# Optimization experiments

Measured on AMD Instinct MI355X. Metric: run time of the kernel, lower is better.

The kernel has to match this reference:

```python
import jax, jax.numpy as jnp
import numpy as np

DIM = 768
N_HEADS = 12
HEAD_DIM = DIM // N_HEADS
B, S = 2, 4096


def setup_inputs() -> dict:
    key = jax.random.key(0)
    k_x, k_wqkv, k_bqkv, k_wout, k_bout = jax.random.split(key, 5)
    scale_in = 1.0 / np.sqrt(DIM)
    return {
        "x": jax.random.normal(k_x, (B, S, DIM), dtype=jnp.float32),
        "Wqkv": jax.random.normal(k_wqkv, (DIM, 3 * DIM), dtype=jnp.float32) * scale_in,
        "bqkv": jax.random.normal(k_bqkv, (3 * DIM,), dtype=jnp.float32) * 0.02,
        "Wout": jax.random.normal(k_wout, (DIM, DIM), dtype=jnp.float32) * scale_in,
        "bout": jax.random.normal(k_bout, (DIM,), dtype=jnp.float32) * 0.02,
    }


def reference(x, Wqkv, bqkv, Wout, bout):
    b, s, d = x.shape
    qkv = (x @ Wqkv + bqkv).reshape(b, s, 3, N_HEADS, HEAD_DIM)
    qkv = jnp.transpose(qkv, (2, 0, 3, 1, 4))  # [3, B, H, S, hd]
    q, k, v = qkv[0], qkv[1], qkv[2]
    scale = HEAD_DIM ** -0.5
    attn = jnp.einsum('bhqd,bhkd->bhqk', q, k) * scale  # [B, H, S, S]
    causal_mask = jnp.triu(jnp.ones((s, s), dtype=bool), k=1)
    attn = jnp.where(causal_mask[None, None], -jnp.inf, attn)
    attn = jax.nn.softmax(attn, axis=-1)
    out = jnp.einsum('bhqk,bhkd->bhqd', attn, v)  # [B, H, S, hd]
    out = jnp.transpose(out, (0, 2, 1, 3)).reshape(b, s, d)
    return out @ Wout + bout
```

## Files before the change

kernel.cpp:

```cpp
#include <hip/hip_runtime.h>
#include <hip/hip_bf16.h>
#include <math.h>

#define DIM 768
#define NH 12
#define HD 64
#define BATCH 2
#define SEQ 4096
#define MTOT (BATCH * SEQ)

#define QSCALE 0.1803368801111244f

typedef unsigned short u16;
typedef __bf16 bf16x8 __attribute__((ext_vector_type(8)));
typedef float  f32x4  __attribute__((ext_vector_type(4)));
typedef unsigned short u16x4 __attribute__((ext_vector_type(4)));
typedef unsigned short u16x8 __attribute__((ext_vector_type(8)));

__device__ inline u16 f2bf(float f) {
    unsigned u = __builtin_bit_cast(unsigned, f);
    u += 0x7fffu + ((u >> 16) & 1u);
    return (u16)(u >> 16);
}

#if defined(__has_builtin) && __has_builtin(__builtin_amdgcn_cvt_pk_bf16_f32)
#define HAVE_PK_BF16 1
__device__ inline unsigned pk2bf(float a, float b) {
    auto v = __builtin_amdgcn_cvt_pk_bf16_f32(a, b);
    return __builtin_bit_cast(unsigned, v);
}
#else
#define HAVE_PK_BF16 0
__device__ inline unsigned pk2bf(float a, float b) {
    return (unsigned)f2bf(a) | ((unsigned)f2bf(b) << 16);
}
#endif

__device__ inline f32x4 mfma16(bf16x8 a, bf16x8 b, f32x4 c) {
    return __builtin_amdgcn_mfma_f32_16x16x32_bf16(a, b, c, 0, 0, 0);
}

__device__ inline void gl2lds16(const u16* g, u16* l) {
    __builtin_amdgcn_global_load_lds(
        (const __attribute__((address_space(1))) void*)g,
        (__attribute__((address_space(3))) void*)l,
        16, 0, 0);
}

__global__ __launch_bounds__(256)
void cvt_bf16(const float* __restrict__ src, u16* __restrict__ dst, int n8)
{
    int i = blockIdx.x * 256 + threadIdx.x;
    if (i >= n8) return;
    float4 a = ((const float4*)src)[i * 2];
    float4 b = ((const float4*)src)[i * 2 + 1];
    u16x8 o;
    o[0] = f2bf(a.x); o[1] = f2bf(a.y); o[2] = f2bf(a.z); o[3] = f2bf(a.w);
    o[4] = f2bf(b.x); o[5] = f2bf(b.y); o[6] = f2bf(b.z); o[7] = f2bf(b.w);
    ((u16x8*)dst)[i] = o;
}

__global__ __launch_bounds__(256)
void transpose_to_bf16(const float* __restrict__ src, u16* __restrict__ dst,
                       int R, int C)
{
    __shared__ float tile[32][33];
    const int c0 = blockIdx.x * 32, r0 = blockIdx.y * 32;
    const int tx = threadIdx.x & 31, ty = threadIdx.x >> 5;
#pragma unroll
    for (int i = 0; i < 4; ++i) {
        int row = ty * 4 + i;
        tile[row][tx] = src[(size_t)(r0 + row) * C + c0 + tx];
    }
    __syncthreads();
#pragma unroll
    for (int i = 0; i < 4; ++i) {
        int crow = ty * 4 + i;
        dst[(size_t)(c0 + crow) * R + r0 + tx] = f2bf(tile[tx][crow]);
    }
}

__device__ inline void gemm_lds_mainloop(const u16* __restrict__ Ag,
                                         const u16* __restrict__ Bg,
                                         int m0, int n0, int w, int lane,
                                         u16 (*As)[64 * 64], u16 (*Bs)[64 * 64],
                                         f32x4 acc[4][4])
{
    const int quad = lane >> 4, lc = lane & 15;
    const int wm = (w & 1) * 64, wn = (w >> 1) * 64;
    const int drow = lane >> 3;
    const int dp   = lane & 7;

#pragma unroll
    for (int mi = 0; mi < 4; ++mi)
#pragma unroll
        for (int nj = 0; nj < 4; ++nj)
            acc[mi][nj] = f32x4{0.f, 0.f, 0.f, 0.f};

#pragma unroll
    for (int i = 0; i < 2; ++i) {
        const int r  = w * 16 + i * 8 + drow;
        const int g  = dp ^ (r & 7);
        const int tr = 2 * r + (g >> 2);
        const int kc = g & 3;
        gl2lds16(Ag + (size_t)(m0 + tr) * 768 + kc * 8, &As[0][(w * 16 + i * 8) * 64]);
        gl2lds16(Bg + (size_t)(n0 + tr) * 768 + kc * 8, &Bs[0][(w * 16 + i * 8) * 64]);
    }
    __syncthreads();

    for (int ks = 0; ks < 24; ++ks) {
        const int cur = ks & 1;

        if (ks < 23) {
            const int k0n = (ks + 1) * 32;
#pragma unroll
            for (int i = 0; i < 2; ++i) {
                const int r  = w * 16 + i * 8 + drow;
                const int g  = dp ^ (r & 7);
                const int tr = 2 * r + (g >> 2);
                const int kc = g & 3;
                gl2lds16(Ag + (size_t)(m0 + tr) * 768 + k0n + kc * 8,
                         &As[1 - cur][(w * 16 + i * 8) * 64]);
                gl2lds16(Bg + (size_t)(n0 + tr) * 768 + k0n + kc * 8,
                         &Bs[1 - cur][(w * 16 + i * 8) * 64]);
            }
        }

        bf16x8 af[4], bfr[4];
#pragma unroll
        for (int mi = 0; mi < 4; ++mi) {
            const int m = wm + mi * 16 + lc;
            const int r = m >> 1;
            const int p = (((m & 1) * 4 + quad)) ^ (r & 7);
            af[mi] = *(const bf16x8*)&As[cur][r * 64 + p * 8];
        }
#pragma unroll
        for (int nj = 0; nj < 4; ++nj) {
            const int n = wn + nj * 16 + lc;
            const int r = n >> 1;
            const int p = (((n & 1) * 4 + quad)) ^ (r & 7);
            bfr[nj] = *(const bf16x8*)&Bs[cur][r * 64 + p * 8];
        }

#pragma unroll
        for (int mi = 0; mi < 4; ++mi)
#pragma unroll
            for (int nj = 0; nj < 4; ++nj)
                acc[mi][nj] = mfma16(af[mi], bfr[nj], acc[mi][nj]);

        __syncthreads();
    }
}

__global__ __launch_bounds__(256)
void gemm_qkv_mfma(const u16* __restrict__ A, const u16* __restrict__ Bt,
                   const float* __restrict__ bias,
                   u16* __restrict__ Qb, u16* __restrict__ Kb, u16* __restrict__ Vt)
{
    __shared__ u16 As[2][64 * 64];
    __shared__ u16 Bs[2][64 * 64];
    const int m0 = blockIdx.x * 128;
    const int n0 = blockIdx.y * 128;
    const int t = threadIdx.x;
    const int w = t >> 6, lane = t & 63;
    const int quad = lane >> 4, lc = lane & 15;
    const int wm = (w & 1) * 64, wn = (w >> 1) * 64;

    f32x4 acc[4][4];
    gemm_lds_mainloop(A, Bt, m0, n0, w, lane, As, Bs, acc);

    const int b  = m0 >> 12;
    const int s0 = (m0 & 4095) + wm;
    const int nbase = n0 + wn;
    const int three = nbase / 768;
    const int rem   = nbase - three * 768;
    const int h     = rem >> 6;
    const int bh    = b * NH + h;

    if (three < 2) {
        u16* dst = (three == 0) ? Qb : Kb;
        const float qs = (three == 0) ? QSCALE : 1.0f;
#pragma unroll
        for (int nj = 0; nj < 4; ++nj) {
            const float bi = bias[nbase + nj * 16 + lc];
            const int d = nj * 16 + lc;
#pragma unroll
            for (int mi = 0; mi < 4; ++mi) {
                const int s = s0 + mi * 16 + quad * 4;
#pragma unroll
                for (int r = 0; r < 4; ++r)
                    dst[((size_t)bh * SEQ + s + r) * HD + d] = f2bf((acc[mi][nj][r] + bi) * qs);
            }
        }
    } else {
#pragma unroll
        for (int nj = 0; nj < 4; ++nj) {
            const float bi = bias[nbase + nj * 16 + lc];
            const int d = nj * 16 + lc;
            const size_t rowb = ((size_t)bh * HD + d) * SEQ;
#pragma unroll
            for (int mi = 0; mi < 4; ++mi) {
                const int s = s0 + mi * 16 + quad * 4;
                u16x4 wv;
#pragma unroll
                for (int r = 0; r < 4; ++r) wv[r] = f2bf(acc[mi][nj][r] + bi);
                *(u16x4*)&Vt[rowb + s] = wv;
            }
        }
    }
}

__global__ __launch_bounds__(256)
void gemm_out_mfma(const u16* __restrict__ A, const u16* __restrict__ Bt,
                   const float* __restrict__ bias, float* __restrict__ C)
{
    __shared__ u16 As[2][64 * 64];
    __shared__ u16 Bs[2][64 * 64];
    const int m0 = blockIdx.x * 128;
    const int n0 = blockIdx.y * 128;
    const int t = threadIdx.x;
    const int w = t >> 6, lane = t & 63;
    const int quad = lane >> 4, lc = lane & 15;
    const int wm = (w & 1) * 64, wn = (w >> 1) * 64;

    f32x4 acc[4][4];
    gemm_lds_mainloop(A, Bt, m0, n0, w, lane, As, Bs, acc);

#pragma unroll
    for (int nj = 0; nj < 4; ++nj) {
        const int col = n0 + wn + nj * 16 + lc;
        const float bi = bias[col];
#pragma unroll
        for (int mi = 0; mi < 4; ++mi) {
            const int row = m0 + wm + mi * 16 + quad * 4;
#pragma unroll
            for (int r = 0; r < 4; ++r)
                C[(size_t)(row + r) * 768 + col] = acc[mi][nj][r] + bi;
        }
    }
}

__global__ __launch_bounds__(256)
void flash_attn(const u16* __restrict__ Qg, const u16* __restrict__ Kg,
                const u16* __restrict__ Vtg, u16* __restrict__ Og)
{
    const int bh   = blockIdx.x;
    const int pair = blockIdx.y;
    const int b    = bh / NH, h = bh % NH;
    const int t    = threadIdx.x;
    const int w    = t >> 6;
    const int wq   = w >> 1;
    const int wk   = w & 1;
    const int lane = t & 63;
    const int quad = lane >> 4;
    const int lc   = lane & 15;
    const int drow = lane >> 3;
    const int dp   = lane & 7;

    __shared__ u16 Ks[2][64 * 64];
    __shared__ u16 Vs[2][64 * 64];
    __shared__ u16 Pl[4][32][32];

    const u16* Qp = Qg  + (size_t)bh * SEQ * HD;
    const u16* Kp = Kg  + (size_t)bh * SEQ * HD;
    const u16* Vp = Vtg + (size_t)bh * HD * SEQ;
    float* Vscr = (float*)&Vs[0][0];
    float* Lx   = (float*)&Ks[0][0];

#pragma unroll 1
    for (int half = 0; half < 2; ++half) {
        const int qt    = half ? pair : (63 - pair);
        const int qrow0 = qt * 64 + wq * 32;

        bf16x8 qa[2][2];
#pragma unroll
        for (int mi = 0; mi < 2; ++mi)
#pragma unroll
            for (int hk = 0; hk < 2; ++hk)
                qa[mi][hk] = *(const bf16x8*)
                    &Qp[(size_t)(qrow0 + mi * 16 + lc) * HD + hk * 32 + quad * 8];

        f32x4 o[2][4];
        float l_r[2][4];
#pragma unroll
        for (int mi = 0; mi < 2; ++mi)
#pragma unroll
            for (int nd = 0; nd < 4; ++nd) o[mi][nd] = f32x4{0.f, 0.f, 0.f, 0.f};
#pragma unroll
        for (int mi = 0; mi < 2; ++mi)
#pragma unroll
            for (int r = 0; r < 4; ++r) l_r[mi][r] = 0.f;

#pragma unroll
        for (int i = 0; i < 2; ++i) {
            const int r0  = w * 16 + i * 8;
            const int row = r0 + drow;
            const int gc  = dp ^ (row & 7);
            gl2lds16(Kp + (size_t)row * HD + gc * 8, &Ks[0][r0 * 64]);
            gl2lds16(Vp + (size_t)row * SEQ + gc * 8, &Vs[0][r0 * 64]);
        }
        __syncthreads();

        for (int tk = 0; tk <= qt; ++tk) {
            const int kb  = tk * 64;
            const int cur = tk & 1;

            if (tk < qt) {
                const int kbn = kb + 64;
#pragma unroll
                for (int i = 0; i < 2; ++i) {
                    const int r0  = w * 16 + i * 8;
                    const int row = r0 + drow;
                    const int gc  = dp ^ (row & 7);
                    gl2lds16(Kp + (size_t)(kbn + row) * HD + gc * 8,
                             &Ks[1 - cur][r0 * 64]);
                    gl2lds16(Vp + (size_t)row * SEQ + kbn + gc * 8,
                             &Vs[1 - cur][r0 * 64]);
                }
            }

            bf16x8 kf[2][2];
#pragma unroll
            for (int nj = 0; nj < 2; ++nj) {
                const int row = wk * 32 + nj * 16 + lc;
                const int sw  = row & 7;
#pragma unroll
                for (int hk = 0; hk < 2; ++hk)
                    kf[nj][hk] = *(const bf16x8*)
                        &Ks[cur][row * 64 + ((quad + 4 * hk) ^ sw) * 8];
            }

            f32x4 sacc[2][2];
#pragma unroll
            for (int mi = 0; mi < 2; ++mi)
#pragma unroll
                for (int nj = 0; nj < 2; ++nj) {
                    f32x4 s = f32x4{0.f, 0.f, 0.f, 0.f};
                    s = mfma16(qa[mi][0], kf[nj][0], s);
                    s = mfma16(qa[mi][1], kf[nj][1], s);
                    sacc[mi][nj] = s;
                }

            if (tk == qt) {
#pragma unroll
                for (int mi = 0; mi < 2; ++mi)
#pragma unroll
                    for (int nj = 0; nj < 2; ++nj) {
                        const int key = kb + wk * 32 + nj * 16 + lc;
                        const int qb2 = qrow0 + mi * 16 + quad * 4;
#pragma unroll
                        for (int r = 0; r < 4; ++r)
                            if (key > qb2 + r) sacc[mi][nj][r] = -1e30f;
                    }
            }

#pragma unroll
            for (int mi = 0; mi < 2; ++mi)
#pragma unroll
                for (int nj = 0; nj < 2; ++nj) {
                    float pv[4];
#pragma unroll
                    for (int r = 0; r < 4; ++r) {
                        pv[r] = __builtin_amdgcn_exp2f(sacc[mi][nj][r]);
                        l_r[mi][r] += pv[r];
                    }
                    const unsigned u01 = pk2bf(pv[0], pv[1]);
                    const unsigned u23 = pk2bf(pv[2], pv[3]);
                    const int rowb = mi * 16 + quad * 4;
                    const int cch  = nj * 2 + (lc >> 3);
                    const int cel  = lc & 7;
                    Pl[w][rowb + 0][((cch ^ 0) * 8) + cel] = (u16)(u01 & 0xffff);
                    Pl[w][rowb + 1][((cch ^ 1) * 8) + cel] = (u16)(u01 >> 16);
                    Pl[w][rowb + 2][((cch ^ 2) * 8) + cel] = (u16)(u23 & 0xffff);
                    Pl[w][rowb + 3][((cch ^ 3) * 8) + cel] = (u16)(u23 >> 16);
                }

            bf16x8 pa[2];
#pragma unroll
            for (int mi = 0; mi < 2; ++mi)
                pa[mi] = *(const bf16x8*)
                    &Pl[w][mi * 16 + lc][(quad ^ (lc & 3)) * 8];
#pragma unroll
            for (int nd = 0; nd < 4; ++nd) {
                const int row = nd * 16 + lc;
                const int sw  = row & 7;
                bf16x8 vf = *(const bf16x8*)
                    &Vs[cur][row * 64 + ((wk * 4 + quad) ^ sw) * 8];
                o[0][nd] = mfma16(pa[0], vf, o[0][nd]);
                o[1][nd] = mfma16(pa[1], vf, o[1][nd]);
            }

            __syncthreads();
        }

#pragma unroll
        for (int mi = 0; mi < 2; ++mi)
#pragma unroll
            for (int r = 0; r < 4; ++r) {
                float rs = l_r[mi][r];
                rs += __shfl_xor(rs, 1);
                rs += __shfl_xor(rs, 2);
                rs += __shfl_xor(rs, 4);
                rs += __shfl_xor(rs, 8);
                l_r[mi][r] = rs;
            }

        if (wk == 1) {
#pragma unroll
            for (int mi = 0; mi < 2; ++mi)
#pragma unroll
                for (int nd = 0; nd < 4; ++nd)
#pragma unroll
                    for (int r = 0; r < 4; ++r)
                        Vscr[wq * 2048 + (mi * 16 + quad * 4 + r) * 64 + nd * 16 + lc]
                            = o[mi][nd][r];
            if (lc == 0) {
#pragma unroll
                for (int mi = 0; mi < 2; ++mi)
#pragma unroll
                    for (int r = 0; r < 4; ++r)
                        Lx[wq * 32 + mi * 16 + quad * 4 + r] = l_r[mi][r];
            }
        }
        __syncthreads();
        if (wk == 0) {
#pragma unroll
            for (int mi = 0; mi < 2; ++mi)
#pragma unroll
                for (int r = 0; r < 4; ++r) {
                    const int rowl = mi * 16 + quad * 4 + r;
                    const float lsum = l_r[mi][r] + Lx[wq * 32 + rowl];
                    const float inv  = 1.0f / lsum;
                    const int q = qrow0 + rowl;
                    const size_t base = ((size_t)(b * SEQ + q)) * DIM + h * HD + lc;
#pragma unroll
                    for (int nd = 0; nd < 4; ++nd) {
                        const float ov = o[mi][nd][r]
                            + Vscr[wq * 2048 + rowl * 64 + nd * 16 + lc];
                        Og[base + nd * 16] = f2bf(ov * inv);
                    }
                }
        }
        __syncthreads();
    }
}

extern "C" void kernel_launch(void* const* d_in, const int* in_sizes, int n_in,
                              void* d_out, int out_size, void* d_ws, size_t ws_size,
                              hipStream_t stream)
{
    const float* x    = (const float*)d_in[0];
    const float* Wqkv = (const float*)d_in[1];
    const float* bqkv = (const float*)d_in[2];
    const float* Wout = (const float*)d_in[3];
    const float* bout = (const float*)d_in[4];
    float* out = (float*)d_out;

    const size_t NX  = (size_t)MTOT * DIM;
    const size_t NWQ = (size_t)DIM * 3 * DIM;
    const size_t NWO = (size_t)DIM * DIM;
    u16* p   = (u16*)d_ws;
    u16* Xb  = p;              p += NX;
    u16* Wqt = p;              p += NWQ;
    u16* Wot = p;              p += NWO;
    u16* Qb  = p;              p += NX;
    u16* Kb  = p;              p += NX;
    u16* Vt  = p;              p += NX;
    u16* Ao  = p;

    cvt_bf16<<<(int)(NX / 8 + 255) / 256, 256, 0, stream>>>(x, Xb, (int)(NX / 8));
    transpose_to_bf16<<<dim3(2304 / 32, 768 / 32), 256, 0, stream>>>(Wqkv, Wqt, 768, 2304);
    transpose_to_bf16<<<dim3(768 / 32, 768 / 32), 256, 0, stream>>>(Wout, Wot, 768, 768);

    gemm_qkv_mfma<<<dim3(MTOT / 128, 2304 / 128), 256, 0, stream>>>(Xb, Wqt, bqkv, Qb, Kb, Vt);
    flash_attn<<<dim3(24, 32), 256, 0, stream>>>(Qb, Kb, Vt, Ao);
    gemm_out_mfma<<<dim3(MTOT / 128, 768 / 128), 256, 0, stream>>>(Ao, Wot, bout, out);
}
```

Baseline: 253.9 us.

## Use 32x32x16 MFMA with transposed S and permlane swap instead of LDS P staging

Switches the attention inner loop from 16x16x32 MFMAs to 32x32x16 MFMAs and computes S transposed (K as the A operand), so each lane owns one query row. The P tile is built for the PV MFMA in registers with v_permlane32_swap, which removes the per-wave LDS scratch and its writes and reads. The row-sum reduction shrinks to a single cross-half shuffle. It also adds an occupancy hint of 3 blocks per CU, which may raise register pressure or cause spills.

Result: faster. 243.0 us (-4.3%).

```diff
diff --git a/kernel.cpp b/kernel.cpp
--- a/kernel.cpp
+++ b/kernel.cpp
@@ -14,8 +14,10 @@
 typedef unsigned short u16;
 typedef __bf16 bf16x8 __attribute__((ext_vector_type(8)));
 typedef float  f32x4  __attribute__((ext_vector_type(4)));
+typedef float  f32x16 __attribute__((ext_vector_type(16)));
 typedef unsigned short u16x4 __attribute__((ext_vector_type(4)));
 typedef unsigned short u16x8 __attribute__((ext_vector_type(8)));
+typedef unsigned u32x4 __attribute__((ext_vector_type(4)));
 
 __device__ inline u16 f2bf(float f) {
     unsigned u = __builtin_bit_cast(unsigned, f);
@@ -38,6 +40,9 @@
 
 __device__ inline f32x4 mfma16(bf16x8 a, bf16x8 b, f32x4 c) {
     return __builtin_amdgcn_mfma_f32_16x16x32_bf16(a, b, c, 0, 0, 0);
+}
+__device__ inline f32x16 mfma32(bf16x8 a, bf16x8 b, f32x16 c) {
+    return __builtin_amdgcn_mfma_f32_32x32x16_bf16(a, b, c, 0, 0, 0);
 }
 
 __device__ inline void gl2lds16(const u16* g, u16* l) {
@@ -240,7 +245,7 @@
     }
 }
 
-__global__ __launch_bounds__(256)
+__global__ __launch_bounds__(256, 3)
 void flash_attn(const u16* __restrict__ Qg, const u16* __restrict__ Kg,
                 const u16* __restrict__ Vtg, u16* __restrict__ Og)
 {
@@ -252,14 +257,13 @@
     const int wq   = w >> 1;
     const int wk   = w & 1;
     const int lane = t & 63;
-    const int quad = lane >> 4;
-    const int lc   = lane & 15;
+    const int lc32 = lane & 31;
+    const int hi   = lane >> 5;
     const int drow = lane >> 3;
     const int dp   = lane & 7;
 
     __shared__ u16 Ks[2][64 * 64];
     __shared__ u16 Vs[2][64 * 64];
-    __shared__ u16 Pl[4][32][32];
 
     const u16* Qp = Qg  + (size_t)bh * SEQ * HD;
     const u16* Kp = Kg  + (size_t)bh * SEQ * HD;
@@ -272,24 +276,16 @@
         const int qt    = half ? pair : (63 - pair);
         const int qrow0 = qt * 64 + wq * 32;
 
-        bf16x8 qa[2][2];
-#pragma unroll
-        for (int mi = 0; mi < 2; ++mi)
-#pragma unroll
-            for (int hk = 0; hk < 2; ++hk)
-                qa[mi][hk] = *(const bf16x8*)
-                    &Qp[(size_t)(qrow0 + mi * 16 + lc) * HD + hk * 32 + quad * 8];
-
-        f32x4 o[2][4];
-        float l_r[2][4];
-#pragma unroll
-        for (int mi = 0; mi < 2; ++mi)
-#pragma unroll
-            for (int nd = 0; nd < 4; ++nd) o[mi][nd] = f32x4{0.f, 0.f, 0.f, 0.f};
-#pragma unroll
-        for (int mi = 0; mi < 2; ++mi)
-#pragma unroll
-            for (int r = 0; r < 4; ++r) l_r[mi][r] = 0.f;
+        bf16x8 qa[4];
+#pragma unroll
+        for (int ds = 0; ds < 4; ++ds)
+            qa[ds] = *(const bf16x8*)
+                &Qp[(size_t)(qrow0 + lc32) * HD + ds * 16 + hi * 8];
+
+        f32x16 o2[2];
+        o2[0] = f32x16{};
+        o2[1] = f32x16{};
+        float l_r = 0.f;
 
 #pragma unroll
         for (int i = 0; i < 2; ++i) {
@@ -319,127 +315,94 @@
                 }
             }
 
-            bf16x8 kf[2][2];
-#pragma unroll
-            for (int nj = 0; nj < 2; ++nj) {
-                const int row = wk * 32 + nj * 16 + lc;
+            f32x16 sacc = {};
+            {
+                const int row = wk * 32 + lc32;
                 const int sw  = row & 7;
 #pragma unroll
-                for (int hk = 0; hk < 2; ++hk)
-                    kf[nj][hk] = *(const bf16x8*)
-                        &Ks[cur][row * 64 + ((quad + 4 * hk) ^ sw) * 8];
-            }
-
-            f32x4 sacc[2][2];
-#pragma unroll
-            for (int mi = 0; mi < 2; ++mi)
-#pragma unroll
-                for (int nj = 0; nj < 2; ++nj) {
-                    f32x4 s = f32x4{0.f, 0.f, 0.f, 0.f};
-                    s = mfma16(qa[mi][0], kf[nj][0], s);
-                    s = mfma16(qa[mi][1], kf[nj][1], s);
-                    sacc[mi][nj] = s;
-                }
+                for (int ds = 0; ds < 4; ++ds) {
+                    bf16x8 kf = *(const bf16x8*)
+                        &Ks[cur][row * 64 + (((ds * 2 + hi) ^ sw) * 8)];
+                    sacc = mfma32(kf, qa[ds], sacc);
+                }
+            }
 
             if (tk == qt) {
-#pragma unroll
-                for (int mi = 0; mi < 2; ++mi)
-#pragma unroll
-                    for (int nj = 0; nj < 2; ++nj) {
-                        const int key = kb + wk * 32 + nj * 16 + lc;
-                        const int qb2 = qrow0 + mi * 16 + quad * 4;
-#pragma unroll
-                        for (int r = 0; r < 4; ++r)
-                            if (key > qb2 + r) sacc[mi][nj][r] = -1e30f;
-                    }
-            }
-
-#pragma unroll
-            for (int mi = 0; mi < 2; ++mi)
-#pragma unroll
-                for (int nj = 0; nj < 2; ++nj) {
-                    float pv[4];
-#pragma unroll
-                    for (int r = 0; r < 4; ++r) {
-                        pv[r] = __builtin_amdgcn_exp2f(sacc[mi][nj][r]);
-                        l_r[mi][r] += pv[r];
-                    }
-                    const unsigned u01 = pk2bf(pv[0], pv[1]);
-                    const unsigned u23 = pk2bf(pv[2], pv[3]);
-                    const int rowb = mi * 16 + quad * 4;
-                    const int cch  = nj * 2 + (lc >> 3);
-                    const int cel  = lc & 7;
-                    Pl[w][rowb + 0][((cch ^ 0) * 8) + cel] = (u16)(u01 & 0xffff);
-                    Pl[w][rowb + 1][((cch ^ 1) * 8) + cel] = (u16)(u01 >> 16);
-                    Pl[w][rowb + 2][((cch ^ 2) * 8) + cel] = (u16)(u23 & 0xffff);
-                    Pl[w][rowb + 3][((cch ^ 3) * 8) + cel] = (u16)(u23 >> 16);
-                }
+                const int q = qrow0 + lc32;
+#pragma unroll
+                for (int r = 0; r < 16; ++r) {
+                    const int key = kb + wk * 32 + (r & 3) + 8 * (r >> 2) + 4 * hi;
+                    if (key > q) sacc[r] = -1e30f;
+                }
+            }
+
+            float pv[16];
+#pragma unroll
+            for (int r = 0; r < 16; ++r)
+                pv[r] = __builtin_amdgcn_exp2f(sacc[r]);
+
+            l_r += (((pv[0] + pv[1]) + (pv[2] + pv[3]))
+                  + ((pv[4] + pv[5]) + (pv[6] + pv[7])))
+                 + (((pv[8] + pv[9]) + (pv[10] + pv[11]))
+                  + ((pv[12] + pv[13]) + (pv[14] + pv[15])));
 
             bf16x8 pa[2];
 #pragma unroll
-            for (int mi = 0; mi < 2; ++mi)
-                pa[mi] = *(const bf16x8*)
-                    &Pl[w][mi * 16 + lc][(quad ^ (lc & 3)) * 8];
-#pragma unroll
-            for (int nd = 0; nd < 4; ++nd) {
-                const int row = nd * 16 + lc;
+            for (int s = 0; s < 2; ++s) {
+                unsigned w0 = pk2bf(pv[8 * s + 0], pv[8 * s + 1]);
+                unsigned w1 = pk2bf(pv[8 * s + 2], pv[8 * s + 3]);
+                unsigned w2 = pk2bf(pv[8 * s + 4], pv[8 * s + 5]);
+                unsigned w3 = pk2bf(pv[8 * s + 6], pv[8 * s + 7]);
+                asm("v_permlane32_swap_b32 %0, %1" : "+v"(w0), "+v"(w2));
+                asm("v_permlane32_swap_b32 %0, %1" : "+v"(w1), "+v"(w3));
+                u32x4 tw;
+                tw[0] = w0; tw[1] = w1; tw[2] = w2; tw[3] = w3;
+                pa[s] = __builtin_bit_cast(bf16x8, tw);
+            }
+
+#pragma unroll
+            for (int dt = 0; dt < 2; ++dt) {
+                const int row = dt * 32 + lc32;
                 const int sw  = row & 7;
-                bf16x8 vf = *(const bf16x8*)
-                    &Vs[cur][row * 64 + ((wk * 4 + quad) ^ sw) * 8];
-                o[0][nd] = mfma16(pa[0], vf, o[0][nd]);
-                o[1][nd] = mfma16(pa[1], vf, o[1][nd]);
+#pragma unroll
+                for (int s = 0; s < 2; ++s) {
+                    bf16x8 vf = *(const bf16x8*)
+                        &Vs[cur][row * 64 + (((wk * 4 + s * 2 + hi) ^ sw) * 8)];
+                    o2[dt] = mfma32(pa[s], vf, o2[dt]);
+                }
             }
 
             __syncthreads();
         }
 
-#pragma unroll
-        for (int mi = 0; mi < 2; ++mi)
-#pragma unroll
-            for (int r = 0; r < 4; ++r) {
-                float rs = l_r[mi][r];
-                rs += __shfl_xor(rs, 1);
-                rs += __shfl_xor(rs, 2);
-                rs += __shfl_xor(rs, 4);
-                rs += __shfl_xor(rs, 8);
-                l_r[mi][r] = rs;
-            }
+        const float lt = l_r + __shfl_xor(l_r, 32);
 
         if (wk == 1) {
 #pragma unroll
-            for (int mi = 0; mi < 2; ++mi)
-#pragma unroll
-                for (int nd = 0; nd < 4; ++nd)
-#pragma unroll
-                    for (int r = 0; r < 4; ++r)
-                        Vscr[wq * 2048 + (mi * 16 + quad * 4 + r) * 64 + nd * 16 + lc]
-                            = o[mi][nd][r];
-            if (lc == 0) {
-#pragma unroll
-                for (int mi = 0; mi < 2; ++mi)
-#pragma unroll
-                    for (int r = 0; r < 4; ++r)
-                        Lx[wq * 32 + mi * 16 + quad * 4 + r] = l_r[mi][r];
-            }
+            for (int dt = 0; dt < 2; ++dt)
+#pragma unroll
+                for (int r = 0; r < 16; ++r) {
+                    const int ql = (r & 3) + 8 * (r >> 2) + 4 * hi;
+                    Vscr[wq * 2048 + ql * 64 + dt * 32 + lc32] = o2[dt][r];
+                }
+            if (lane < 32) Lx[wq * 32 + lc32] = lt;
         }
         __syncthreads();
         if (wk == 0) {
-#pragma unroll
-            for (int mi = 0; mi < 2; ++mi)
-#pragma unroll
-                for (int r = 0; r < 4; ++r) {
-                    const int rowl = mi * 16 + quad * 4 + r;
-                    const float lsum = l_r[mi][r] + Lx[wq * 32 + rowl];
-                    const float inv  = 1.0f / lsum;
-                    const int q = qrow0 + rowl;
-                    const size_t base = ((size_t)(b * SEQ + q)) * DIM + h * HD + lc;
-#pragma unroll
-                    for (int nd = 0; nd < 4; ++nd) {
-                        const float ov = o[mi][nd][r]
-                            + Vscr[wq * 2048 + rowl * 64 + nd * 16 + lc];
-                        Og[base + nd * 16] = f2bf(ov * inv);
-                    }
-                }
+            const float linv_q = 1.0f / (lt + Lx[wq * 32 + lc32]);
+#pragma unroll
+            for (int r = 0; r < 16; ++r) {
+                const int ql   = (r & 3) + 8 * (r >> 2) + 4 * hi;
+                const float li = __shfl(linv_q, ql);
+                const int q = qrow0 + ql;
+                const size_t base = ((size_t)(b * SEQ + q)) * DIM + h * HD + lc32;
+#pragma unroll
+                for (int dt = 0; dt < 2; ++dt) {
+                    const float ov = o2[dt][r]
+                        + Vscr[wq * 2048 + ql * 64 + dt * 32 + lc32];
+                    Og[base + dt * 32] = f2bf(ov * li);
+                }
+            }
         }
         __syncthreads();
     }
```
